# Kernel optimization log

Hardware: AMD Instinct MI355X
Metric: run time of the kernel (lower is better)

Reference implementation:

```python
import jax, jax.numpy as jnp
import numpy as np

HOLE_P = 0.05      # fraction of NaN (invalid) pixels
N_PROP = 8         # fixed propagation iterations for hole filling
DOWN_LIMIT = 512   # original code downsamples masks when max dim > 512

# cv2.getStructuringElement(cv2.MORPH_ELLIPSE, (3,3)) is the 4-neighbor cross
_CROSS = np.array([[0., 1., 0.], [1., 1., 1.], [0., 1., 0.]], np.float32)


def _conv_cross_hw(x):
    """3x3 cross conv on a single [H, W] map, zero padding."""
    k = jnp.asarray(_CROSS)[None, None]  # [1,1,3,3]
    y = jax.lax.conv_general_dilated(x[None, None], k, (1, 1), 'SAME',
                                     dimension_numbers=('NCHW', 'OIHW', 'NCHW'))
    return y[0, 0]


def _conv_cross_chw(x):
    """Depthwise 3x3 cross conv on [C, H, W], zero padding."""
    c = x.shape[0]
    k = jnp.tile(jnp.asarray(_CROSS)[None, None], (c, 1, 1, 1))  # [C,1,3,3]
    y = jax.lax.conv_general_dilated(x[None], k, (1, 1), 'SAME',
                                     feature_group_count=c,
                                     dimension_numbers=('NCHW', 'OIHW', 'NCHW'))
    return y[0]


def _dilated_union_mask(invalid_f):
    """Replicates the tri-branch: F.conv2d with weight [1,C,3,3] sums over
    channels (union of per-class invalid masks), then clamps to [0,1].
    When max dim > 512 it nearest-downsamples by dr, dilates, and nearest-
    upsamples back. invalid_f: [C,H,W] float -> [H,W] float in {0,1}."""
    c, h, w = invalid_f.shape
    s = invalid_f.sum(0)  # channel sum == conv over channel dim
    m = max(c, h, w)
    if m > DOWN_LIMIT:
        dr = m / DOWN_LIMIT
        hs, ws = int(h / dr), int(w / dr)
        # nearest downsample: index floor(i * h / hs)
        ri = (jnp.arange(hs) * h // hs).astype(jnp.int32)
        ci = (jnp.arange(ws) * w // ws).astype(jnp.int32)
        s_small = s[ri][:, ci]
        d_small = jnp.clip(_conv_cross_hw(s_small), 0.0, 1.0)
        # nearest upsample back to (h, w)
        ri_up = (jnp.arange(h) * hs // h).astype(jnp.int32)
        ci_up = (jnp.arange(w) * ws // w).astype(jnp.int32)
        d = d_small[ri_up][:, ci_up]
    else:
        d = jnp.clip(_conv_cross_hw(s), 0.0, 1.0)
    return d


def _fill_missing(x, invalid):
    """NaN-free formulation of fillMissingValues_tensor (tri mode).
    x: [C,H,W] float values; invalid: [C,H,W] bool (pixels that were NaN).
    Source pixels = valid pixels adjacent to the dilated union invalid mask
    (plus the 4 image corners, as in the original corner fixup). Invalid
    pixels are filled by iterative 4-neighbor weighted propagation from the
    source set (GPU-native stand-in for the Interp2D triangulated fill)."""
    invalid_f = invalid.astype(jnp.float32)
    dil = _dilated_union_mask(invalid_f)                       # [H,W]
    src = (dil[None] * (1.0 - invalid_f))                      # [C,H,W]
    # corner fixup: *0 then +1 -> forced to 1
    for (i, j) in [(0, 0), (0, -1), (-1, 0), (-1, -1)]:
        src = src.at[:, i, j].set(1.0)
    v = jnp.where(src > 0, jnp.where(invalid, 0.0, x), 0.0)
    w = jnp.where(src > 0, 1.0, 0.0)

    def step(carry, _):
        v, w = carry
        nv = _conv_cross_chw(v)
        nw = _conv_cross_chw(w)
        new = (w == 0.0) & (nw > 0.0)
        v = jnp.where(new, nv / jnp.maximum(nw, 1e-6), v)
        w = jnp.where(new, 1.0, w)
        return (v, w), None

    (v, w), _ = jax.lax.scan(step, (v, w), None, length=N_PROP)
    # replace only the invalid pixels (original keeps valid pixels untouched)
    return jnp.where(invalid, v, x)


def setup_inputs() -> dict:
    key = jax.random.key(0)
    k1, k2 = jax.random.split(key)
    x = jax.random.normal(k1, (16, 1024, 1024), dtype=jnp.float32)
    hole_u = jax.random.uniform(k2, (16, 1024, 1024), dtype=jnp.float32)
    return {"x": x, "hole_u": hole_u}


def reference(x, hole_u):
    invalid = hole_u < HOLE_P  # models torch.isnan(target_for_interp)
    return _fill_missing(x, invalid)
```

## Files before the change

kernel.cpp:

```cpp
#include <hip/hip_runtime.h>

#define HOLE_P 0.05f
#define TW 64
#define TH 64
#define HALO 8
#define PRW 88
#define PRH 82
#define PLN 7216
#define PWORDS 1804
#define QCAP 1536

__global__ void k_mask(const float* __restrict__ hole_u, unsigned char* __restrict__ inv_mask) {
    int t = blockIdx.x * blockDim.x + threadIdx.x;
    const float* base = hole_u + (size_t)t * 8;
    float4 a = *reinterpret_cast<const float4*>(base);
    float4 b = *reinterpret_cast<const float4*>(base + 4);
    unsigned int m = (a.x < HOLE_P ? 1u : 0u)  | (a.y < HOLE_P ? 2u : 0u)  |
                     (a.z < HOLE_P ? 4u : 0u)  | (a.w < HOLE_P ? 8u : 0u)  |
                     (b.x < HOLE_P ? 16u : 0u) | (b.y < HOLE_P ? 32u : 0u) |
                     (b.z < HOLE_P ? 64u : 0u) | (b.w < HOLE_P ? 128u : 0u);
    inv_mask[t] = (unsigned char)m;
}

__global__ void k_us(const unsigned char* __restrict__ inv_mask, unsigned char* __restrict__ u_small) {
    int t = blockIdx.x * blockDim.x + threadIdx.x;
    int i  = t >> 7;
    int jb = t & 127;
    const unsigned char* p = inv_mask + (i << 8) + jb;
    unsigned int b = 0;
#pragma unroll
    for (int c = 0; c < 16; ++c) b |= p[c * 131072];
    unsigned int o = (b & 1u) | (((b >> 2) & 1u) << 8) | (((b >> 4) & 1u) << 16) | (((b >> 6) & 1u) << 24);
    *reinterpret_cast<unsigned int*>(u_small + i * 512 + jb * 4) = o;
}

__global__ void k_dil(const unsigned char* __restrict__ u_small, unsigned char* __restrict__ d_small) {
    int g = blockIdx.x * blockDim.x + threadIdx.x;
    int i = g >> 9, j = g & 511;
    unsigned char d = u_small[g];
    if (i > 0)   d |= u_small[g - 512];
    if (i < 511) d |= u_small[g + 512];
    if (j > 0)   d |= u_small[g - 1];
    if (j < 511) d |= u_small[g + 1];
    d_small[g] = d;
}

__device__ __forceinline__ void halo_map(int h, int& ly, int& lxg) {
    if (h < 160)      { ly = h / 20;                lxg = h - (h / 20) * 20; }
    else if (h < 320) { int t2 = h - 160; ly = 72 + t2 / 20; lxg = t2 - (t2 / 20) * 20; }
    else              { int t2 = h - 320; ly = 8 + (t2 >> 2); int q = t2 & 3; lxg = q < 2 ? q : q + 16; }
}

__device__ __forceinline__ unsigned int enc_w(unsigned int src, unsigned int nib) {
    return ((src * 0x204081u) & 0x01010101u) | (((nib * 0x204081u) & 0x01010101u) << 7);
}

__global__ __launch_bounds__(512, 4) void k_fill(
    const float* __restrict__ x, const unsigned char* __restrict__ inv_mask,
    const unsigned char* __restrict__ d_small, float* __restrict__ out)
{
    __shared__ __align__(16) float v[PLN];
    __shared__ unsigned int w32[PWORDS];
    __shared__ unsigned short q[QCAP];
    __shared__ int qn;
    __shared__ int chgf[8], pendf[8];
    unsigned char* w = (unsigned char*)w32;

    const int tid = threadIdx.x;
    const int c   = blockIdx.z;
    const int by0 = blockIdx.y * TH;
    const int bx0 = blockIdx.x * TW;
    const float* xc = x + c * 1048576;
    const unsigned char* mc = inv_mask + c * 131072;
    float* oc = out + c * 1048576;
    const bool cornerTile = ((blockIdx.x == 0) | (blockIdx.x == 15)) &
                            ((blockIdx.y == 0) | (blockIdx.y == 15));

    if (tid < 8) { chgf[tid] = 0; pendf[tid] = 0; }
    if (tid == 0) qn = 0;
    if (tid < 204) {
        int wi;
        if (tid < 22)      wi = tid;
        else if (tid < 44) wi = 81 * 22 + (tid - 22);
        else {
            int r = ((tid - 44) >> 1) + 1;
            wi = r * 22 + (((tid - 44) & 1) ? 21 : 0);
        }
        w32[wi] = 0x7f7f7f7fu;
    }
    __syncthreads();

    int r0  = tid >> 4, cg0 = tid & 15;
    int gy0 = by0 + r0,      gx0 = bx0 + cg0 * 4;
    int gy1 = by0 + r0 + 32;
    float4 xx0 = *reinterpret_cast<const float4*>(xc + gy0 * 1024 + gx0);
    float4 xx1 = *reinterpret_cast<const float4*>(xc + gy1 * 1024 + gx0);
    unsigned int mb0 = mc[(gy0 << 7) + (gx0 >> 3)];
    unsigned int mb1 = mc[(gy1 << 7) + (gx0 >> 3)];
    unsigned short dsA = *reinterpret_cast<const unsigned short*>(d_small + ((gy0 >> 1) << 9) + (gx0 >> 1));
    unsigned short dsB = *reinterpret_cast<const unsigned short*>(d_small + ((gy1 >> 1) << 9) + (gx0 >> 1));

    int aly, alxg, bly, blxg;
    halo_map(tid, aly, alxg);
    const bool hasB = (tid < 64);
    halo_map(hasB ? tid + 512 : 0, bly, blxg);
    int agy  = by0 - HALO + aly,  agx0 = bx0 - HALO + alxg * 4;
    int bgy  = by0 - HALO + bly,  bgx0 = bx0 - HALO + blxg * 4;
    bool ain = ((unsigned)agy < 1024u) & ((unsigned)agx0 < 1024u);
    bool bin = hasB & ((unsigned)bgy < 1024u) & ((unsigned)bgx0 < 1024u);
    float4 axx = make_float4(0.f, 0.f, 0.f, 0.f), bxx = axx;
    unsigned int amb = 0, bmb = 0; unsigned short ads = 0, bds = 0;
    if (ain) {
        int gi = agy * 1024 + agx0;
        axx = *reinterpret_cast<const float4*>(xc + gi);
        amb = mc[(agy << 7) + (agx0 >> 3)];
        ads = *reinterpret_cast<const unsigned short*>(d_small + ((agy >> 1) << 9) + (agx0 >> 1));
    }
    if (bin) {
        int gi = bgy * 1024 + bgx0;
        bxx = *reinterpret_cast<const float4*>(xc + gi);
        bmb = mc[(bgy << 7) + (bgx0 >> 3)];
        bds = *reinterpret_cast<const unsigned short*>(d_small + ((bgy >> 1) << 9) + (bgx0 >> 1));
    }

    float4 xr[2] = {xx0, xx1};
    unsigned int fN0, fN1, fNA = 0, fNB = 0;
    unsigned int iN0, iN1, iNA = 0, iNB = 0;
    int P0i0, P0i1, P0A, P0B;
    {
        unsigned int nib = (mb0 >> (gx0 & 7)) & 0xfu;
        unsigned int db = ((dsA & 0xffu) ? 0x3u : 0u) | ((dsA & 0xff00u) ? 0xcu : 0u);
        unsigned int src = db & ~nib & 0xfu;
        if (cornerTile && ((gy0 == 0) | (gy0 == 1023)))
            src |= (gx0 == 0 ? 1u : 0u) | (gx0 == 1020 ? 8u : 0u);
        unsigned int vs = src & ~nib;
        float4 vv;
        vv.x = (vs & 1u) ? xx0.x : 0.0f;
        vv.y = (vs & 2u) ? xx0.y : 0.0f;
        vv.z = (vs & 4u) ? xx0.z : 0.0f;
        vv.w = (vs & 8u) ? xx0.w : 0.0f;
        P0i0 = (9 + r0) * PRW + 12 + cg0 * 4;
        *reinterpret_cast<float4*>(&v[P0i0]) = vv;
        w32[P0i0 >> 2] = enc_w(src, nib);
        fN0 = ~src & 0xfu; iN0 = nib;
    }
    {
        unsigned int nib = (mb1 >> (gx0 & 7)) & 0xfu;
        unsigned int db = ((dsB & 0xffu) ? 0x3u : 0u) | ((dsB & 0xff00u) ? 0xcu : 0u);
        unsigned int src = db & ~nib & 0xfu;
        if (cornerTile && ((gy1 == 0) | (gy1 == 1023)))
            src |= (gx0 == 0 ? 1u : 0u) | (gx0 == 1020 ? 8u : 0u);
        unsigned int vs = src & ~nib;
        float4 vv;
        vv.x = (vs & 1u) ? xx1.x : 0.0f;
        vv.y = (vs & 2u) ? xx1.y : 0.0f;
        vv.z = (vs & 4u) ? xx1.z : 0.0f;
        vv.w = (vs & 8u) ? xx1.w : 0.0f;
        P0i1 = (9 + r0 + 32) * PRW + 12 + cg0 * 4;
        *reinterpret_cast<float4*>(&v[P0i1]) = vv;
        w32[P0i1 >> 2] = enc_w(src, nib);
        fN1 = ~src & 0xfu; iN1 = nib;
    }
    {
        P0A = (aly + 1) * PRW + 4 + alxg * 4;
        float4 vv = make_float4(0.f, 0.f, 0.f, 0.f);
        unsigned int ww = 0x7f7f7f7fu;
        if (ain) {
            unsigned int nib = (amb >> (agx0 & 7)) & 0xfu;
            unsigned int db = ((ads & 0xffu) ? 0x3u : 0u) | ((ads & 0xff00u) ? 0xcu : 0u);
            unsigned int src = db & ~nib & 0xfu;
            ww = enc_w(src, nib);
            vv.x = (src & 1u) ? axx.x : 0.0f;
            vv.y = (src & 2u) ? axx.y : 0.0f;
            vv.z = (src & 4u) ? axx.z : 0.0f;
            vv.w = (src & 8u) ? axx.w : 0.0f;
            fNA = ~src & 0xfu; iNA = nib;
        }
        *reinterpret_cast<float4*>(&v[P0A]) = vv;
        w32[P0A >> 2] = ww;
    }
    P0B = (bly + 1) * PRW + 4 + blxg * 4;
    if (hasB) {
        float4 vv = make_float4(0.f, 0.f, 0.f, 0.f);
        unsigned int ww = 0x7f7f7f7fu;
        if (bin) {
            unsigned int nib = (bmb >> (bgx0 & 7)) & 0xfu;
            unsigned int db = ((bds & 0xffu) ? 0x3u : 0u) | ((bds & 0xff00u) ? 0xcu : 0u);
            unsigned int src = db & ~nib & 0xfu;
            ww = enc_w(src, nib);
            vv.x = (src & 1u) ? bxx.x : 0.0f;
            vv.y = (src & 2u) ? bxx.y : 0.0f;
            vv.z = (src & 4u) ? bxx.z : 0.0f;
            vv.w = (src & 8u) ? bxx.w : 0.0f;
            fNB = ~src & 0xfu; iNB = nib;
        }
        *reinterpret_cast<float4*>(&v[P0B]) = vv;
        w32[P0B >> 2] = ww;
    }

    int cnt = __popc(fN0) + __popc(fN1) + __popc(fNA) + __popc(fNB);
    int lane = tid & 63;
    int xsum = cnt;
#pragma unroll
    for (int d = 1; d < 64; d <<= 1) {
        int y = __shfl_up(xsum, d, 64);
        if (lane >= d) xsum += y;
    }
    int base = 0;
    if (lane == 63) base = atomicAdd(&qn, xsum);
    base = __shfl(base, 63, 64);
    int idx = base + (xsum - cnt);
#define PUSH(m_, iv_, pd_, gp_) { unsigned int m = (m_); while (m) {            \
        int b = __builtin_ctz(m); m &= m - 1;                                   \
        unsigned int e = (unsigned int)((gp_) + b) | ((((iv_) >> b) & 1u) << 14)\
                         | ((((pd_) >> b) & 1u) << 15);                         \
        if (idx < QCAP) q[idx] = (unsigned short)e; ++idx; } }
    PUSH(fN0, iN0, fN0 & iN0, P0i0)
    PUSH(fN1, iN1, fN1 & iN1, P0i1)
    PUSH(fNA, iNA, 0u, P0A)
    PUSH(fNB, iNB, 0u, P0B)
#undef PUSH
    __syncthreads();

    const int n = qn;
    if (n <= QCAP) {
        for (int it = 0; it < 8; ++it) {
            int chg = 0, pend = 0;
            unsigned int thr = (unsigned int)it;
            for (int i = tid; i < n; i += 512) {
                unsigned int e = q[i];
                int p = e & 0x1fffu;
                if (w[p] & 0x7fu) continue;
                unsigned int qu = w[p - PRW] & 0x7fu;
                unsigned int qd = w[p + PRW] & 0x7fu;
                unsigned int ql = w[p - 1]   & 0x7fu;
                unsigned int qr = w[p + 1]   & 0x7fu;
                bool su = (qu - 1u) <= thr, sd = (qd - 1u) <= thr;
                bool sl = (ql - 1u) <= thr, sr = (qr - 1u) <= thr;
                float s = (su ? v[p - PRW] : 0.0f) + (sd ? v[p + PRW] : 0.0f)
                        + (sl ? v[p - 1]   : 0.0f) + (sr ? v[p + 1]   : 0.0f);
                int cn = (int)su + (int)sd + (int)sl + (int)sr;
                if (cn > 0) {
                    v[p] = s / (float)cn;
                    w[p] = (unsigned char)((((e >> 14) & 1u) << 7) | (unsigned int)(it + 2));
                    chg = 1;
                } else {
                    pend |= (int)((e >> 15) & 1u);
                }
            }
            if (chg)  chgf[it] = 1;
            if (pend) pendf[it] = 1;
            __syncthreads();
            if (chgf[it] == 0 || pendf[it] == 0) break;
        }
    } else {
        for (int it = 0; it < 8; ++it) {
            int chg = 0;
            unsigned int thr = (unsigned int)it;
            for (int wp = tid; wp < PWORDS; wp += 512) {
                unsigned int cw = w32[wp];
                unsigned int st = cw & 0x7f7f7f7fu;
                if ((((st - 0x01010101u) & ~st) & 0x80808080u) == 0u) continue;
                int p0 = wp * 4;
#pragma unroll
                for (int b = 0; b < 4; ++b) {
                    if (((st >> (8 * b)) & 0x7fu) != 0u) continue;
                    int p = p0 + b;
                    unsigned int qu = w[p - PRW] & 0x7fu, qd = w[p + PRW] & 0x7fu;
                    unsigned int ql = w[p - 1] & 0x7fu,   qr = w[p + 1] & 0x7fu;
                    bool su = (qu - 1u) <= thr, sd = (qd - 1u) <= thr;
                    bool sl = (ql - 1u) <= thr, sr = (qr - 1u) <= thr;
                    float s = (su ? v[p - PRW] : 0.0f) + (sd ? v[p + PRW] : 0.0f)
                            + (sl ? v[p - 1]   : 0.0f) + (sr ? v[p + 1]   : 0.0f);
                    int cn = (int)su + (int)sd + (int)sl + (int)sr;
                    if (cn > 0) {
                        v[p] = s / (float)cn;
                        w[p] = (unsigned char)(((cw >> (8 * b)) & 0x80u) | (unsigned int)(it + 2));
                        chg = 1;
                    }
                }
            }
            if (chg) chgf[it] = 1;
            __syncthreads();
            if (chgf[it] == 0) break;
        }
    }

#pragma unroll
    for (int k = 0; k < 2; ++k) {
        int r  = r0 + k * 32;
        int p0 = (9 + r) * PRW + 12 + cg0 * 4;
        unsigned int cw = w32[p0 >> 2];
        float4 vv = *reinterpret_cast<const float4*>(&v[p0]);
        float4 xx = xr[k];
        float4 o;
        o.x = (cw & 0x00000080u) ? vv.x : xx.x;
        o.y = (cw & 0x00008000u) ? vv.y : xx.y;
        o.z = (cw & 0x00800000u) ? vv.z : xx.z;
        o.w = (cw & 0x80000000u) ? vv.w : xx.w;
        *reinterpret_cast<float4*>(oc + (by0 + r) * 1024 + bx0 + cg0 * 4) = o;
    }
}

extern "C" void kernel_launch(void* const* d_in, const int* in_sizes, int n_in,
                              void* d_out, int out_size, void* d_ws, size_t ws_size,
                              hipStream_t stream) {
    (void)in_sizes; (void)n_in; (void)out_size; (void)ws_size;
    const float* x      = (const float*)d_in[0];
    const float* hole_u = (const float*)d_in[1];
    float* out = (float*)d_out;
    unsigned char* u_small  = (unsigned char*)d_ws;
    unsigned char* d_small  = u_small + 262144;
    unsigned char* inv_mask = d_small + 262144;

    k_mask<<<8192, 256, 0, stream>>>(hole_u, inv_mask);
    k_us  <<<256, 256, 0, stream>>>(inv_mask, u_small);
    k_dil <<<1024, 256, 0, stream>>>(u_small, d_small);
    dim3 grid(16, 16, 16);
    k_fill<<<grid, 512, 0, stream>>>(x, inv_mask, d_small, out);
}
```

Baseline: 54.36 us.

## Make k_fill persistent over four tiles with register prefetch of next tile

k_fill now launches 1024 blocks, and each block handles four tiles in sequence. While the current tile's values are written to shared memory and propagated, the next tile's x, mask and dilation data are loaded into registers. This is meant to hide global load latency behind the propagation loop and to reduce block launch overhead. In exchange it raises register pressure under launch_bounds(512,4) and adds a barrier per tile, and with fewer blocks per CU there is less parallelism to hide latency.

```diff
diff --git a/kernel.cpp b/kernel.cpp
--- a/kernel.cpp
+++ b/kernel.cpp
@@ -9,6 +9,8 @@
 #define PLN 7216
 #define PWORDS 1804
 #define QCAP 1536
+#define NTILES 4
+#define NBLK 1024
 
 __global__ void k_mask(const float* __restrict__ hole_u, unsigned char* __restrict__ inv_mask) {
     int t = blockIdx.x * blockDim.x + threadIdx.x;
@@ -55,6 +57,58 @@
     return ((src * 0x204081u) & 0x01010101u) | (((nib * 0x204081u) & 0x01010101u) << 7);
 }
 
+struct TR {
+    float4 xx0, xx1, axx, bxx;
+    unsigned int mb0, mb1, amb, bmb;
+    unsigned int dsA, dsB, ads, bds;
+    int by0, bx0;
+    const float* xc;
+    float* oc;
+    bool ain, bin, cornerTile;
+};
+
+__device__ __forceinline__ void tile_load(
+    const float* __restrict__ x, const unsigned char* __restrict__ inv_mask,
+    const unsigned char* __restrict__ d_small, float* __restrict__ out,
+    int tileId, int r0, int cg0, int aly, int alxg, int bly, int blxg, bool hasB,
+    TR& R)
+{
+    int c  = tileId >> 8;
+    int ty = (tileId >> 4) & 15;
+    int tx = tileId & 15;
+    R.by0 = ty * TH; R.bx0 = tx * TW;
+    R.xc = x + c * 1048576;
+    R.oc = out + c * 1048576;
+    const unsigned char* mc = inv_mask + c * 131072;
+    R.cornerTile = ((tx == 0) | (tx == 15)) & ((ty == 0) | (ty == 15));
+    int gy0 = R.by0 + r0, gx0 = R.bx0 + cg0 * 4;
+    int gy1 = gy0 + 32;
+    R.xx0 = *reinterpret_cast<const float4*>(R.xc + gy0 * 1024 + gx0);
+    R.xx1 = *reinterpret_cast<const float4*>(R.xc + gy1 * 1024 + gx0);
+    R.mb0 = mc[(gy0 << 7) + (gx0 >> 3)];
+    R.mb1 = mc[(gy1 << 7) + (gx0 >> 3)];
+    R.dsA = *reinterpret_cast<const unsigned short*>(d_small + ((gy0 >> 1) << 9) + (gx0 >> 1));
+    R.dsB = *reinterpret_cast<const unsigned short*>(d_small + ((gy1 >> 1) << 9) + (gx0 >> 1));
+    int agy = R.by0 - HALO + aly, agx0 = R.bx0 - HALO + alxg * 4;
+    int bgy = R.by0 - HALO + bly, bgx0 = R.bx0 - HALO + blxg * 4;
+    R.ain = ((unsigned)agy < 1024u) & ((unsigned)agx0 < 1024u);
+    R.bin = hasB & ((unsigned)bgy < 1024u) & ((unsigned)bgx0 < 1024u);
+    R.axx = make_float4(0.f, 0.f, 0.f, 0.f); R.bxx = R.axx;
+    R.amb = 0; R.bmb = 0; R.ads = 0; R.bds = 0;
+    if (R.ain) {
+        int gi = agy * 1024 + agx0;
+        R.axx = *reinterpret_cast<const float4*>(R.xc + gi);
+        R.amb = mc[(agy << 7) + (agx0 >> 3)];
+        R.ads = *reinterpret_cast<const unsigned short*>(d_small + ((agy >> 1) << 9) + (agx0 >> 1));
+    }
+    if (R.bin) {
+        int gi = bgy * 1024 + bgx0;
+        R.bxx = *reinterpret_cast<const float4*>(R.xc + gi);
+        R.bmb = mc[(bgy << 7) + (bgx0 >> 3)];
+        R.bds = *reinterpret_cast<const unsigned short*>(d_small + ((bgy >> 1) << 9) + (bgx0 >> 1));
+    }
+}
+
 __global__ __launch_bounds__(512, 4) void k_fill(
     const float* __restrict__ x, const unsigned char* __restrict__ inv_mask,
     const unsigned char* __restrict__ d_small, float* __restrict__ out)
@@ -67,17 +121,17 @@
     unsigned char* w = (unsigned char*)w32;
 
     const int tid = threadIdx.x;
-    const int c   = blockIdx.z;
-    const int by0 = blockIdx.y * TH;
-    const int bx0 = blockIdx.x * TW;
-    const float* xc = x + c * 1048576;
-    const unsigned char* mc = inv_mask + c * 131072;
-    float* oc = out + c * 1048576;
-    const bool cornerTile = ((blockIdx.x == 0) | (blockIdx.x == 15)) &
-                            ((blockIdx.y == 0) | (blockIdx.y == 15));
-
-    if (tid < 8) { chgf[tid] = 0; pendf[tid] = 0; }
-    if (tid == 0) qn = 0;
+    const int lane = tid & 63;
+    const int r0  = tid >> 4, cg0 = tid & 15;
+    int aly, alxg, bly, blxg;
+    halo_map(tid, aly, alxg);
+    const bool hasB = (tid < 64);
+    halo_map(hasB ? tid + 512 : 0, bly, blxg);
+    const int P0i0 = (9 + r0) * PRW + 12 + cg0 * 4;
+    const int P0i1 = P0i0 + 32 * PRW;
+    const int P0A  = (aly + 1) * PRW + 4 + alxg * 4;
+    const int P0B  = (bly + 1) * PRW + 4 + blxg * 4;
+
     if (tid < 204) {
         int wi;
         if (tid < 22)      wi = tid;
@@ -88,186 +142,132 @@
         }
         w32[wi] = 0x7f7f7f7fu;
     }
+    if (tid < 8) { chgf[tid] = 0; pendf[tid] = 0; }
+    if (tid == 0) qn = 0;
+
+    TR R[2];
+    tile_load(x, inv_mask, d_small, out, blockIdx.x,
+              r0, cg0, aly, alxg, bly, blxg, hasB, R[0]);
     __syncthreads();
 
-    int r0  = tid >> 4, cg0 = tid & 15;
-    int gy0 = by0 + r0,      gx0 = bx0 + cg0 * 4;
-    int gy1 = by0 + r0 + 32;
-    float4 xx0 = *reinterpret_cast<const float4*>(xc + gy0 * 1024 + gx0);
-    float4 xx1 = *reinterpret_cast<const float4*>(xc + gy1 * 1024 + gx0);
-    unsigned int mb0 = mc[(gy0 << 7) + (gx0 >> 3)];
-    unsigned int mb1 = mc[(gy1 << 7) + (gx0 >> 3)];
-    unsigned short dsA = *reinterpret_cast<const unsigned short*>(d_small + ((gy0 >> 1) << 9) + (gx0 >> 1));
-    unsigned short dsB = *reinterpret_cast<const unsigned short*>(d_small + ((gy1 >> 1) << 9) + (gx0 >> 1));
-
-    int aly, alxg, bly, blxg;
-    halo_map(tid, aly, alxg);
-    const bool hasB = (tid < 64);
-    halo_map(hasB ? tid + 512 : 0, bly, blxg);
-    int agy  = by0 - HALO + aly,  agx0 = bx0 - HALO + alxg * 4;
-    int bgy  = by0 - HALO + bly,  bgx0 = bx0 - HALO + blxg * 4;
-    bool ain = ((unsigned)agy < 1024u) & ((unsigned)agx0 < 1024u);
-    bool bin = hasB & ((unsigned)bgy < 1024u) & ((unsigned)bgx0 < 1024u);
-    float4 axx = make_float4(0.f, 0.f, 0.f, 0.f), bxx = axx;
-    unsigned int amb = 0, bmb = 0; unsigned short ads = 0, bds = 0;
-    if (ain) {
-        int gi = agy * 1024 + agx0;
-        axx = *reinterpret_cast<const float4*>(xc + gi);
-        amb = mc[(agy << 7) + (agx0 >> 3)];
-        ads = *reinterpret_cast<const unsigned short*>(d_small + ((agy >> 1) << 9) + (agx0 >> 1));
-    }
-    if (bin) {
-        int gi = bgy * 1024 + bgx0;
-        bxx = *reinterpret_cast<const float4*>(xc + gi);
-        bmb = mc[(bgy << 7) + (bgx0 >> 3)];
-        bds = *reinterpret_cast<const unsigned short*>(d_small + ((bgy >> 1) << 9) + (bgx0 >> 1));
-    }
-
-    float4 xr[2] = {xx0, xx1};
-    unsigned int fN0, fN1, fNA = 0, fNB = 0;
-    unsigned int iN0, iN1, iNA = 0, iNB = 0;
-    int P0i0, P0i1, P0A, P0B;
-    {
-        unsigned int nib = (mb0 >> (gx0 & 7)) & 0xfu;
-        unsigned int db = ((dsA & 0xffu) ? 0x3u : 0u) | ((dsA & 0xff00u) ? 0xcu : 0u);
-        unsigned int src = db & ~nib & 0xfu;
-        if (cornerTile && ((gy0 == 0) | (gy0 == 1023)))
-            src |= (gx0 == 0 ? 1u : 0u) | (gx0 == 1020 ? 8u : 0u);
-        unsigned int vs = src & ~nib;
-        float4 vv;
-        vv.x = (vs & 1u) ? xx0.x : 0.0f;
-        vv.y = (vs & 2u) ? xx0.y : 0.0f;
-        vv.z = (vs & 4u) ? xx0.z : 0.0f;
-        vv.w = (vs & 8u) ? xx0.w : 0.0f;
-        P0i0 = (9 + r0) * PRW + 12 + cg0 * 4;
-        *reinterpret_cast<float4*>(&v[P0i0]) = vv;
-        w32[P0i0 >> 2] = enc_w(src, nib);
-        fN0 = ~src & 0xfu; iN0 = nib;
-    }
-    {
-        unsigned int nib = (mb1 >> (gx0 & 7)) & 0xfu;
-        unsigned int db = ((dsB & 0xffu) ? 0x3u : 0u) | ((dsB & 0xff00u) ? 0xcu : 0u);
-        unsigned int src = db & ~nib & 0xfu;
-        if (cornerTile && ((gy1 == 0) | (gy1 == 1023)))
-            src |= (gx0 == 0 ? 1u : 0u) | (gx0 == 1020 ? 8u : 0u);
-        unsigned int vs = src & ~nib;
-        float4 vv;
-        vv.x = (vs & 1u) ? xx1.x : 0.0f;
-        vv.y = (vs & 2u) ? xx1.y : 0.0f;
-        vv.z = (vs & 4u) ? xx1.z : 0.0f;
-        vv.w = (vs & 8u) ? xx1.w : 0.0f;
-        P0i1 = (9 + r0 + 32) * PRW + 12 + cg0 * 4;
-        *reinterpret_cast<float4*>(&v[P0i1]) = vv;
-        w32[P0i1 >> 2] = enc_w(src, nib);
-        fN1 = ~src & 0xfu; iN1 = nib;
-    }
-    {
-        P0A = (aly + 1) * PRW + 4 + alxg * 4;
-        float4 vv = make_float4(0.f, 0.f, 0.f, 0.f);
-        unsigned int ww = 0x7f7f7f7fu;
-        if (ain) {
-            unsigned int nib = (amb >> (agx0 & 7)) & 0xfu;
-            unsigned int db = ((ads & 0xffu) ? 0x3u : 0u) | ((ads & 0xff00u) ? 0xcu : 0u);
+#pragma unroll
+    for (int t = 0; t < NTILES; ++t) {
+        TR& C = R[t & 1];
+
+        unsigned int fN0, fN1, fNA = 0, fNB = 0;
+        unsigned int iN0, iN1, iNA = 0, iNB = 0;
+        int gx0 = C.bx0 + cg0 * 4;
+        {
+            int gy0 = C.by0 + r0;
+            unsigned int nib = (C.mb0 >> (gx0 & 7)) & 0xfu;
+            unsigned int db = ((C.dsA & 0xffu) ? 0x3u : 0u) | ((C.dsA & 0xff00u) ? 0xcu : 0u);
             unsigned int src = db & ~nib & 0xfu;
-            ww = enc_w(src, nib);
-            vv.x = (src & 1u) ? axx.x : 0.0f;
-            vv.y = (src & 2u) ? axx.y : 0.0f;
-            vv.z = (src & 4u) ? axx.z : 0.0f;
-            vv.w = (src & 8u) ? axx.w : 0.0f;
-            fNA = ~src & 0xfu; iNA = nib;
-        }
-        *reinterpret_cast<float4*>(&v[P0A]) = vv;
-        w32[P0A >> 2] = ww;
-    }
-    P0B = (bly + 1) * PRW + 4 + blxg * 4;
-    if (hasB) {
-        float4 vv = make_float4(0.f, 0.f, 0.f, 0.f);
-        unsigned int ww = 0x7f7f7f7fu;
-        if (bin) {
-            unsigned int nib = (bmb >> (bgx0 & 7)) & 0xfu;
-            unsigned int db = ((bds & 0xffu) ? 0x3u : 0u) | ((bds & 0xff00u) ? 0xcu : 0u);
+            if (C.cornerTile && ((gy0 == 0) | (gy0 == 1023)))
+                src |= (gx0 == 0 ? 1u : 0u) | (gx0 == 1020 ? 8u : 0u);
+            unsigned int vs = src & ~nib;
+            float4 vv;
+            vv.x = (vs & 1u) ? C.xx0.x : 0.0f;
+            vv.y = (vs & 2u) ? C.xx0.y : 0.0f;
+            vv.z = (vs & 4u) ? C.xx0.z : 0.0f;
+            vv.w = (vs & 8u) ? C.xx0.w : 0.0f;
+            *reinterpret_cast<float4*>(&v[P0i0]) = vv;
+            w32[P0i0 >> 2] = enc_w(src, nib);
+            fN0 = ~src & 0xfu; iN0 = nib;
+        }
+        {
+            int gy1 = C.by0 + r0 + 32;
+            unsigned int nib = (C.mb1 >> (gx0 & 7)) & 0xfu;
+            unsigned int db = ((C.dsB & 0xffu) ? 0x3u : 0u) | ((C.dsB & 0xff00u) ? 0xcu : 0u);
             unsigned int src = db & ~nib & 0xfu;
-            ww = enc_w(src, nib);
-            vv.x = (src & 1u) ? bxx.x : 0.0f;
-            vv.y = (src & 2u) ? bxx.y : 0.0f;
-            vv.z = (src & 4u) ? bxx.z : 0.0f;
-            vv.w = (src & 8u) ? bxx.w : 0.0f;
-            fNB = ~src & 0xfu; iNB = nib;
-        }
-        *reinterpret_cast<float4*>(&v[P0B]) = vv;
-        w32[P0B >> 2] = ww;
-    }
-
-    int cnt = __popc(fN0) + __popc(fN1) + __popc(fNA) + __popc(fNB);
-    int lane = tid & 63;
-    int xsum = cnt;
-#pragma unroll
-    for (int d = 1; d < 64; d <<= 1) {
-        int y = __shfl_up(xsum, d, 64);
-        if (lane >= d) xsum += y;
-    }
-    int base = 0;
-    if (lane == 63) base = atomicAdd(&qn, xsum);
-    base = __shfl(base, 63, 64);
-    int idx = base + (xsum - cnt);
+            if (C.cornerTile && ((gy1 == 0) | (gy1 == 1023)))
+                src |= (gx0 == 0 ? 1u : 0u) | (gx0 == 1020 ? 8u : 0u);
+            unsigned int vs = src & ~nib;
+            float4 vv;
+            vv.x = (vs & 1u) ? C.xx1.x : 0.0f;
+            vv.y = (vs & 2u) ? C.xx1.y : 0.0f;
+            vv.z = (vs & 4u) ? C.xx1.z : 0.0f;
+            vv.w = (vs & 8u) ? C.xx1.w : 0.0f;
+            *reinterpret_cast<float4*>(&v[P0i1]) = vv;
+            w32[P0i1 >> 2] = enc_w(src, nib);
+            fN1 = ~src & 0xfu; iN1 = nib;
+        }
+        {
+            int agx0 = C.bx0 - HALO + alxg * 4;
+            float4 vv = make_float4(0.f, 0.f, 0.f, 0.f);
+            unsigned int ww = 0x7f7f7f7fu;
+            if (C.ain) {
+                unsigned int nib = (C.amb >> (agx0 & 7)) & 0xfu;
+                unsigned int db = ((C.ads & 0xffu) ? 0x3u : 0u) | ((C.ads & 0xff00u) ? 0xcu : 0u);
+                unsigned int src = db & ~nib & 0xfu;
+                ww = enc_w(src, nib);
+                vv.x = (src & 1u) ? C.axx.x : 0.0f;
+                vv.y = (src & 2u) ? C.axx.y : 0.0f;
+                vv.z = (src & 4u) ? C.axx.z : 0.0f;
+                vv.w = (src & 8u) ? C.axx.w : 0.0f;
+                fNA = ~src & 0xfu; iNA = nib;
+            }
+            *reinterpret_cast<float4*>(&v[P0A]) = vv;
+            w32[P0A >> 2] = ww;
+        }
+        if (hasB) {
+            int bgx0 = C.bx0 - HALO + blxg * 4;
+            float4 vv = make_float4(0.f, 0.f, 0.f, 0.f);
+            unsigned int ww = 0x7f7f7f7fu;
+            if (C.bin) {
+                unsigned int nib = (C.bmb >> (bgx0 & 7)) & 0xfu;
+                unsigned int db = ((C.bds & 0xffu) ? 0x3u : 0u) | ((C.bds & 0xff00u) ? 0xcu : 0u);
+                unsigned int src = db & ~nib & 0xfu;
+                ww = enc_w(src, nib);
+                vv.x = (src & 1u) ? C.bxx.x : 0.0f;
+                vv.y = (src & 2u) ? C.bxx.y : 0.0f;
+                vv.z = (src & 4u) ? C.bxx.z : 0.0f;
+                vv.w = (src & 8u) ? C.bxx.w : 0.0f;
+                fNB = ~src & 0xfu; iNB = nib;
+            }
+            *reinterpret_cast<float4*>(&v[P0B]) = vv;
+            w32[P0B >> 2] = ww;
+        }
+
+        if (t + 1 < NTILES)
+            tile_load(x, inv_mask, d_small, out, (t + 1) * NBLK + blockIdx.x,
+                      r0, cg0, aly, alxg, bly, blxg, hasB, R[(t + 1) & 1]);
+
+        int cnt = __popc(fN0) + __popc(fN1) + __popc(fNA) + __popc(fNB);
+        int xsum = cnt;
+#pragma unroll
+        for (int d = 1; d < 64; d <<= 1) {
+            int y = __shfl_up(xsum, d, 64);
+            if (lane >= d) xsum += y;
+        }
+        int base = 0;
+        if (lane == 63) base = atomicAdd(&qn, xsum);
+        base = __shfl(base, 63, 64);
+        int idx = base + (xsum - cnt);
 #define PUSH(m_, iv_, pd_, gp_) { unsigned int m = (m_); while (m) {            \
         int b = __builtin_ctz(m); m &= m - 1;                                   \
         unsigned int e = (unsigned int)((gp_) + b) | ((((iv_) >> b) & 1u) << 14)\
                          | ((((pd_) >> b) & 1u) << 15);                         \
         if (idx < QCAP) q[idx] = (unsigned short)e; ++idx; } }
-    PUSH(fN0, iN0, fN0 & iN0, P0i0)
-    PUSH(fN1, iN1, fN1 & iN1, P0i1)
-    PUSH(fNA, iNA, 0u, P0A)
-    PUSH(fNB, iNB, 0u, P0B)
+        PUSH(fN0, iN0, fN0 & iN0, P0i0)
+        PUSH(fN1, iN1, fN1 & iN1, P0i1)
+        PUSH(fNA, iNA, 0u, P0A)
+        PUSH(fNB, iNB, 0u, P0B)
 #undef PUSH
-    __syncthreads();
-
-    const int n = qn;
-    if (n <= QCAP) {
-        for (int it = 0; it < 8; ++it) {
-            int chg = 0, pend = 0;
-            unsigned int thr = (unsigned int)it;
-            for (int i = tid; i < n; i += 512) {
-                unsigned int e = q[i];
-                int p = e & 0x1fffu;
-                if (w[p] & 0x7fu) continue;
-                unsigned int qu = w[p - PRW] & 0x7fu;
-                unsigned int qd = w[p + PRW] & 0x7fu;
-                unsigned int ql = w[p - 1]   & 0x7fu;
-                unsigned int qr = w[p + 1]   & 0x7fu;
-                bool su = (qu - 1u) <= thr, sd = (qd - 1u) <= thr;
-                bool sl = (ql - 1u) <= thr, sr = (qr - 1u) <= thr;
-                float s = (su ? v[p - PRW] : 0.0f) + (sd ? v[p + PRW] : 0.0f)
-                        + (sl ? v[p - 1]   : 0.0f) + (sr ? v[p + 1]   : 0.0f);
-                int cn = (int)su + (int)sd + (int)sl + (int)sr;
-                if (cn > 0) {
-                    v[p] = s / (float)cn;
-                    w[p] = (unsigned char)((((e >> 14) & 1u) << 7) | (unsigned int)(it + 2));
-                    chg = 1;
-                } else {
-                    pend |= (int)((e >> 15) & 1u);
-                }
-            }
-            if (chg)  chgf[it] = 1;
-            if (pend) pendf[it] = 1;
-            __syncthreads();
-            if (chgf[it] == 0 || pendf[it] == 0) break;
-        }
-    } else {
-        for (int it = 0; it < 8; ++it) {
-            int chg = 0;
-            unsigned int thr = (unsigned int)it;
-            for (int wp = tid; wp < PWORDS; wp += 512) {
-                unsigned int cw = w32[wp];
-                unsigned int st = cw & 0x7f7f7f7fu;
-                if ((((st - 0x01010101u) & ~st) & 0x80808080u) == 0u) continue;
-                int p0 = wp * 4;
-#pragma unroll
-                for (int b = 0; b < 4; ++b) {
-                    if (((st >> (8 * b)) & 0x7fu) != 0u) continue;
-                    int p = p0 + b;
-                    unsigned int qu = w[p - PRW] & 0x7fu, qd = w[p + PRW] & 0x7fu;
-                    unsigned int ql = w[p - 1] & 0x7fu,   qr = w[p + 1] & 0x7fu;
+        __syncthreads();
+
+        const int n = qn;
+        if (n <= QCAP) {
+            for (int it = 0; it < 8; ++it) {
+                int chg = 0, pend = 0;
+                unsigned int thr = (unsigned int)it;
+                for (int i = tid; i < n; i += 512) {
+                    unsigned int e = q[i];
+                    int p = e & 0x1fffu;
+                    if (w[p] & 0x7fu) continue;
+                    unsigned int qu = w[p - PRW] & 0x7fu;
+                    unsigned int qd = w[p + PRW] & 0x7fu;
+                    unsigned int ql = w[p - 1]   & 0x7fu;
+                    unsigned int qr = w[p + 1]   & 0x7fu;
                     bool su = (qu - 1u) <= thr, sd = (qd - 1u) <= thr;
                     bool sl = (ql - 1u) <= thr, sr = (qr - 1u) <= thr;
                     float s = (su ? v[p - PRW] : 0.0f) + (sd ? v[p + PRW] : 0.0f)
@@ -275,30 +275,70 @@
                     int cn = (int)su + (int)sd + (int)sl + (int)sr;
                     if (cn > 0) {
                         v[p] = s / (float)cn;
-                        w[p] = (unsigned char)(((cw >> (8 * b)) & 0x80u) | (unsigned int)(it + 2));
+                        w[p] = (unsigned char)((((e >> 14) & 1u) << 7) | (unsigned int)(it + 2));
                         chg = 1;
+                    } else {
+                        pend |= (int)((e >> 15) & 1u);
                     }
                 }
+                if (chg)  chgf[it] = 1;
+                if (pend) pendf[it] = 1;
+                __syncthreads();
+                if (chgf[it] == 0 || pendf[it] == 0) break;
             }
-            if (chg) chgf[it] = 1;
+        } else {
+            for (int it = 0; it < 8; ++it) {
+                int chg = 0;
+                unsigned int thr = (unsigned int)it;
+                for (int wp = tid; wp < PWORDS; wp += 512) {
+                    unsigned int cw = w32[wp];
+                    unsigned int st = cw & 0x7f7f7f7fu;
+                    if ((((st - 0x01010101u) & ~st) & 0x80808080u) == 0u) continue;
+                    int p0 = wp * 4;
+#pragma unroll
+                    for (int b = 0; b < 4; ++b) {
+                        if (((st >> (8 * b)) & 0x7fu) != 0u) continue;
+                        int p = p0 + b;
+                        unsigned int qu = w[p - PRW] & 0x7fu, qd = w[p + PRW] & 0x7fu;
+                        unsigned int ql = w[p - 1] & 0x7fu,   qr = w[p + 1] & 0x7fu;
+                        bool su = (qu - 1u) <= thr, sd = (qd - 1u) <= thr;
+                        bool sl = (ql - 1u) <= thr, sr = (qr - 1u) <= thr;
+                        float s = (su ? v[p - PRW] : 0.0f) + (sd ? v[p + PRW] : 0.0f)
+                                + (sl ? v[p - 1]   : 0.0f) + (sr ? v[p + 1]   : 0.0f);
+                        int cn = (int)su + (int)sd + (int)sl + (int)sr;
+                        if (cn > 0) {
+                            v[p] = s / (float)cn;
+                            w[p] = (unsigned char)(((cw >> (8 * b)) & 0x80u) | (unsigned int)(it + 2));
+                            chg = 1;
+                        }
+                    }
+                }
+                if (chg) chgf[it] = 1;
+                __syncthreads();
+                if (chgf[it] == 0) break;
+            }
+        }
+
+#pragma unroll
+        for (int k = 0; k < 2; ++k) {
+            int r  = r0 + k * 32;
+            int p0 = (9 + r) * PRW + 12 + cg0 * 4;
+            unsigned int cw = w32[p0 >> 2];
+            float4 vv = *reinterpret_cast<const float4*>(&v[p0]);
+            float4 xx = (k == 0) ? C.xx0 : C.xx1;
+            float4 o;
+            o.x = (cw & 0x00000080u) ? vv.x : xx.x;
+            o.y = (cw & 0x00008000u) ? vv.y : xx.y;
+            o.z = (cw & 0x00800000u) ? vv.z : xx.z;
+            o.w = (cw & 0x80000000u) ? vv.w : xx.w;
+            *reinterpret_cast<float4*>(C.oc + (C.by0 + r) * 1024 + C.bx0 + cg0 * 4) = o;
+        }
+
+        if (t + 1 < NTILES) {
+            if (tid < 8) { chgf[tid] = 0; pendf[tid] = 0; }
+            if (tid == 0) qn = 0;
             __syncthreads();
-            if (chgf[it] == 0) break;
-        }
-    }
-
-#pragma unroll
-    for (int k = 0; k < 2; ++k) {
-        int r  = r0 + k * 32;
-        int p0 = (9 + r) * PRW + 12 + cg0 * 4;
-        unsigned int cw = w32[p0 >> 2];
-        float4 vv = *reinterpret_cast<const float4*>(&v[p0]);
-        float4 xx = xr[k];
-        float4 o;
-        o.x = (cw & 0x00000080u) ? vv.x : xx.x;
-        o.y = (cw & 0x00008000u) ? vv.y : xx.y;
-        o.z = (cw & 0x00800000u) ? vv.z : xx.z;
-        o.w = (cw & 0x80000000u) ? vv.w : xx.w;
-        *reinterpret_cast<float4*>(oc + (by0 + r) * 1024 + bx0 + cg0 * 4) = o;
+        }
     }
 }
 
@@ -316,6 +356,5 @@
     k_mask<<<8192, 256, 0, stream>>>(hole_u, inv_mask);
     k_us  <<<256, 256, 0, stream>>>(inv_mask, u_small);
     k_dil <<<1024, 256, 0, stream>>>(u_small, d_small);
-    dim3 grid(16, 16, 16);
-    k_fill<<<grid, 512, 0, stream>>>(x, inv_mask, d_small, out);
-}
+    k_fill<<<NBLK, 512, 0, stream>>>(x, inv_mask, d_small, out);
+}
```

New measurement: 58.75 us. 8.1% more time.
